# Kernel tuning notes

Hardware: AMD Instinct MI355X
Metric: run time of the kernel (lower is better)

The kernel has to match this reference:

```python
import jax, jax.numpy as jnp
import numpy as np

ALPHA = 0.2  # LeakyReLU negative slope
NEG_INF = -9e15


def setup_inputs() -> dict:
    key = jax.random.key(0)
    k1, k2, k3, k4 = jax.random.split(key, 4)
    N, F_in, F_out = 8192, 256, 64
    h = jax.random.normal(k1, (N, F_in), dtype=jnp.float32)
    adj = jax.random.randint(k2, (N, N), 0, 2, dtype=jnp.int32)
    # xavier-uniform-style scaling for params
    W = jax.random.normal(k3, (F_in, F_out), dtype=jnp.float32) * (1.0 / np.sqrt(F_in))
    a = jax.random.normal(k4, (2 * F_out, 1), dtype=jnp.float32) * (1.0 / np.sqrt(F_out))
    return {"h": h, "adj": adj, "W": W, "a": a}


def reference(h, adj, W, a):
    # Wh: [N, F_out]
    Wh = h @ W
    F_out = W.shape[1]
    a1 = a[:F_out, 0]   # attends to source (row i)
    a2 = a[F_out:, 0]   # attends to target (row j)
    f1 = Wh @ a1        # [N]
    f2 = Wh @ a2        # [N]
    # e[i, j] = leakyrelu(Wh_i . a1 + Wh_j . a2)  == original repeat/cat math
    e = jax.nn.leaky_relu(f1[:, None] + f2[None, :], negative_slope=ALPHA)
    attention = jnp.where(adj > 0, e, NEG_INF)
    attention = jax.nn.softmax(attention, axis=1)
    # dropout omitted (eval / deterministic reference)
    h_prime = attention @ Wh  # [N, F_out]
    return jax.nn.elu(h_prime)
```

## Files before the change

kernel.cpp:

```cpp
#include <hip/hip_runtime.h>
#include <hip/hip_bf16.h>
#include <stdint.h>

#define N 8192
#define FIN 256
#define FOUT 64

typedef __attribute__((ext_vector_type(8))) short s8v;
typedef __attribute__((ext_vector_type(4))) float f4v;

__device__ __forceinline__ uint32_t f2bf(float f) {
  uint32_t u = __float_as_uint(f);
  return (u + 0x7FFFu + ((u >> 16) & 1u)) >> 16;
}

__global__ __launch_bounds__(64) void gat_prep(
    const float* __restrict__ h, const float* __restrict__ W,
    const float* __restrict__ a,
    float* __restrict__ f1, float* __restrict__ f2,
    uint16_t* __restrict__ whT)
{
  const int c = threadIdx.x;
  const int i0 = blockIdx.x * 8;
  float acc[8] = {0.f, 0.f, 0.f, 0.f, 0.f, 0.f, 0.f, 0.f};
  #pragma unroll 4
  for (int k = 0; k < FIN; ++k) {
    float wv = W[k * FOUT + c];
    #pragma unroll
    for (int r = 0; r < 8; ++r)
      acc[r] += h[(size_t)(i0 + r) * FIN + k] * wv;
  }
  uint32_t b[8];
  #pragma unroll
  for (int r = 0; r < 8; ++r) b[r] = f2bf(acc[r]);
  int4 pk;
  pk.x = (int)(b[0] | (b[1] << 16));
  pk.y = (int)(b[2] | (b[3] << 16));
  pk.z = (int)(b[4] | (b[5] << 16));
  pk.w = (int)(b[6] | (b[7] << 16));
  *(int4*)(whT + (size_t)c * N + i0) = pk;

  const float a1 = a[c], a2 = a[FOUT + c];
  #pragma unroll
  for (int r = 0; r < 8; ++r) {
    float v1 = acc[r] * a1;
    float v2 = acc[r] * a2;
    #pragma unroll
    for (int m = 32; m > 0; m >>= 1) {
      v1 += __shfl_xor(v1, m, 64);
      v2 += __shfl_xor(v2, m, 64);
    }
    if (c == 0) { f1[i0 + r] = v1; f2[i0 + r] = v2; }
  }
}

__device__ __forceinline__ s8v make_afrag(float f1v, const int* __restrict__ ap,
                                          const float* __restrict__ fp, float& den) {
  int4 c0 = *(const int4*)ap;
  int4 c1 = *(const int4*)(ap + 4);
  float4 g0 = *(const float4*)fp;
  float4 g1 = *(const float4*)(fp + 4);
  float e0 = f1v + g0.x; e0 = fmaxf(e0, 0.2f * e0); float w0 = (c0.x > 0) ? __expf(e0) : 0.f;
  float e1 = f1v + g0.y; e1 = fmaxf(e1, 0.2f * e1); float w1 = (c0.y > 0) ? __expf(e1) : 0.f;
  float e2 = f1v + g0.z; e2 = fmaxf(e2, 0.2f * e2); float w2 = (c0.z > 0) ? __expf(e2) : 0.f;
  float e3 = f1v + g0.w; e3 = fmaxf(e3, 0.2f * e3); float w3 = (c0.w > 0) ? __expf(e3) : 0.f;
  float e4 = f1v + g1.x; e4 = fmaxf(e4, 0.2f * e4); float w4 = (c1.x > 0) ? __expf(e4) : 0.f;
  float e5 = f1v + g1.y; e5 = fmaxf(e5, 0.2f * e5); float w5 = (c1.y > 0) ? __expf(e5) : 0.f;
  float e6 = f1v + g1.z; e6 = fmaxf(e6, 0.2f * e6); float w6 = (c1.z > 0) ? __expf(e6) : 0.f;
  float e7 = f1v + g1.w; e7 = fmaxf(e7, 0.2f * e7); float w7 = (c1.w > 0) ? __expf(e7) : 0.f;
  uint32_t b0 = f2bf(w0), b1 = f2bf(w1), b2 = f2bf(w2), b3 = f2bf(w3);
  uint32_t b4 = f2bf(w4), b5 = f2bf(w5), b6 = f2bf(w6), b7 = f2bf(w7);
  den += __uint_as_float(b0 << 16) + __uint_as_float(b1 << 16)
       + __uint_as_float(b2 << 16) + __uint_as_float(b3 << 16)
       + __uint_as_float(b4 << 16) + __uint_as_float(b5 << 16)
       + __uint_as_float(b6 << 16) + __uint_as_float(b7 << 16);
  union { s8v v; uint32_t u[4]; } r;
  r.u[0] = b0 | (b1 << 16);
  r.u[1] = b2 | (b3 << 16);
  r.u[2] = b4 | (b5 << 16);
  r.u[3] = b6 | (b7 << 16);
  return r.v;
}

__global__ __launch_bounds__(256) void gat_main2(
    const int* __restrict__ adj, const float* __restrict__ f1,
    const float* __restrict__ f2, const uint16_t* __restrict__ whT,
    float* __restrict__ pnum, float* __restrict__ pden)
{
  const int t = threadIdx.x;
  const int wave = t >> 6;
  const int lane = t & 63;
  const int task = blockIdx.x * 4 + wave;
  const int group = task >> 2;
  const int quarter = task & 3;
  const int i0 = group * 16;
  const int jb = quarter * (N / 4);
  const int m  = lane & 15;
  const int kg = lane >> 4;

  const float f1v = f1[i0 + m];
  const int*      ap  = adj + (size_t)(i0 + m) * N + jb + kg * 8;
  const float*    fp  = f2 + jb + kg * 8;
  const uint16_t* bp0 = whT + (size_t)m * N + jb + kg * 8;

  f4v acc0 = {0.f, 0.f, 0.f, 0.f};
  f4v acc1 = acc0, acc2 = acc0, acc3 = acc0;
  float den = 0.f;

  #pragma unroll 2
  for (int jc = 0; jc < (N / 4) / 64; ++jc) {
    const int j0 = jc * 64;
    s8v a0 = make_afrag(f1v, ap + j0,      fp + j0,      den);
    s8v a1 = make_afrag(f1v, ap + j0 + 32, fp + j0 + 32, den);
    const uint16_t* bp = bp0 + j0;
    s8v b00 = *(const s8v*)(bp);
    s8v b01 = *(const s8v*)(bp + 32);
    s8v b10 = *(const s8v*)(bp + 16 * N);
    s8v b11 = *(const s8v*)(bp + 16 * N + 32);
    s8v b20 = *(const s8v*)(bp + 32 * N);
    s8v b21 = *(const s8v*)(bp + 32 * N + 32);
    s8v b30 = *(const s8v*)(bp + 48 * N);
    s8v b31 = *(const s8v*)(bp + 48 * N + 32);
    acc0 = __builtin_amdgcn_mfma_f32_16x16x32_bf16(a0, b00, acc0, 0, 0, 0);
    acc0 = __builtin_amdgcn_mfma_f32_16x16x32_bf16(a1, b01, acc0, 0, 0, 0);
    acc1 = __builtin_amdgcn_mfma_f32_16x16x32_bf16(a0, b10, acc1, 0, 0, 0);
    acc1 = __builtin_amdgcn_mfma_f32_16x16x32_bf16(a1, b11, acc1, 0, 0, 0);
    acc2 = __builtin_amdgcn_mfma_f32_16x16x32_bf16(a0, b20, acc2, 0, 0, 0);
    acc2 = __builtin_amdgcn_mfma_f32_16x16x32_bf16(a1, b21, acc2, 0, 0, 0);
    acc3 = __builtin_amdgcn_mfma_f32_16x16x32_bf16(a0, b30, acc3, 0, 0, 0);
    acc3 = __builtin_amdgcn_mfma_f32_16x16x32_bf16(a1, b31, acc3, 0, 0, 0);
  }

  den += __shfl_xor(den, 16, 64);
  den += __shfl_xor(den, 32, 64);

  float* np = pnum + (size_t)task * (16 * 64);
  #pragma unroll
  for (int r = 0; r < 4; ++r) {
    int row = kg * 4 + r;
    np[row * 64 +      m] = acc0[r];
    np[row * 64 + 16 + m] = acc1[r];
    np[row * 64 + 32 + m] = acc2[r];
    np[row * 64 + 48 + m] = acc3[r];
  }
  if (lane < 16) pden[task * 16 + m] = den;
}

__global__ __launch_bounds__(256) void gat_combine(
    const float* __restrict__ pnum, const float* __restrict__ pden,
    float* __restrict__ out)
{
  const int idx = blockIdx.x * 256 + threadIdx.x;
  const int i = idx >> 6;
  const int c = idx & 63;
  const int g = i >> 4;
  const int r = i & 15;
  const size_t base = (size_t)g * 4 * 1024 + (size_t)r * 64 + c;
  float num = pnum[base] + pnum[base + 1024] + pnum[base + 2048] + pnum[base + 3072];
  const int db = g * 64 + r;
  float den = pden[db] + pden[db + 16] + pden[db + 32] + pden[db + 48];
  float hp = num / den;
  out[idx] = (hp > 0.f) ? hp : (__expf(hp) - 1.f);
}

extern "C" void kernel_launch(void* const* d_in, const int* in_sizes, int n_in,
                              void* d_out, int out_size, void* d_ws, size_t ws_size,
                              hipStream_t stream) {
  const float* h   = (const float*)d_in[0];
  const int*   adj = (const int*)d_in[1];
  const float* W   = (const float*)d_in[2];
  const float* a   = (const float*)d_in[3];
  float* out = (float*)d_out;

  float* f1 = (float*)d_ws;
  float* f2 = f1 + N;
  uint16_t* whT = (uint16_t*)(f2 + N);
  float* pnum = (float*)(whT + (size_t)FOUT * N);
  float* pden = pnum + (size_t)2048 * 16 * 64;

  gat_prep<<<N / 8, 64, 0, stream>>>(h, W, a, f1, f2, whT);
  gat_main2<<<512, 256, 0, stream>>>(adj, f1, f2, whT, pnum, pden);
  gat_combine<<<(N * FOUT) / 256, 256, 0, stream>>>(pnum, pden, out);
}
```

Baseline: 436.9 us.

## Split column range eightfold, prefetch adjacency tiles, widen prep blocks

The main attention kernel now splits each 16-row group's column range into 8 parts instead of 4, doubling the wave count to expose more parallelism for the memory-bound adjacency stream. The adjacency and f2 loads for the next 64-column chunk are software-prefetched into registers one iteration ahead. The prep kernel moves from 64-thread blocks of 8 rows to 256-thread blocks of 4 rows per wave. Partial buffers and the combine reduction grow to 8 partials, which adds workspace traffic and register pressure.

```diff
diff --git a/kernel.cpp b/kernel.cpp
--- a/kernel.cpp
+++ b/kernel.cpp
@@ -5,6 +5,10 @@
 #define N 8192
 #define FIN 256
 #define FOUT 64
+#define QSPLIT 8
+#define NTASK (512 * QSPLIT)
+#define JLEN (N / QSPLIT)
+#define NITER (JLEN / 64)
 
 typedef __attribute__((ext_vector_type(8))) short s8v;
 typedef __attribute__((ext_vector_type(4))) float f4v;
@@ -14,35 +18,32 @@
   return (u + 0x7FFFu + ((u >> 16) & 1u)) >> 16;
 }
 
-__global__ __launch_bounds__(64) void gat_prep(
+__global__ __launch_bounds__(256) void gat_prep(
     const float* __restrict__ h, const float* __restrict__ W,
     const float* __restrict__ a,
     float* __restrict__ f1, float* __restrict__ f2,
     uint16_t* __restrict__ whT)
 {
-  const int c = threadIdx.x;
-  const int i0 = blockIdx.x * 8;
-  float acc[8] = {0.f, 0.f, 0.f, 0.f, 0.f, 0.f, 0.f, 0.f};
-  #pragma unroll 4
+  const int c = threadIdx.x & 63;
+  const int wave = threadIdx.x >> 6;
+  const int i0 = blockIdx.x * 16 + wave * 4;
+  float acc[4] = {0.f, 0.f, 0.f, 0.f};
+  #pragma unroll 8
   for (int k = 0; k < FIN; ++k) {
     float wv = W[k * FOUT + c];
     #pragma unroll
-    for (int r = 0; r < 8; ++r)
+    for (int r = 0; r < 4; ++r)
       acc[r] += h[(size_t)(i0 + r) * FIN + k] * wv;
   }
-  uint32_t b[8];
-  #pragma unroll
-  for (int r = 0; r < 8; ++r) b[r] = f2bf(acc[r]);
-  int4 pk;
-  pk.x = (int)(b[0] | (b[1] << 16));
-  pk.y = (int)(b[2] | (b[3] << 16));
-  pk.z = (int)(b[4] | (b[5] << 16));
-  pk.w = (int)(b[6] | (b[7] << 16));
-  *(int4*)(whT + (size_t)c * N + i0) = pk;
+  uint32_t b0 = f2bf(acc[0]), b1 = f2bf(acc[1]), b2 = f2bf(acc[2]), b3 = f2bf(acc[3]);
+  int2 pk;
+  pk.x = (int)(b0 | (b1 << 16));
+  pk.y = (int)(b2 | (b3 << 16));
+  *(int2*)(whT + (size_t)c * N + i0) = pk;
 
   const float a1 = a[c], a2 = a[FOUT + c];
   #pragma unroll
-  for (int r = 0; r < 8; ++r) {
+  for (int r = 0; r < 4; ++r) {
     float v1 = acc[r] * a1;
     float v2 = acc[r] * a2;
     #pragma unroll
@@ -54,12 +55,8 @@
   }
 }
 
-__device__ __forceinline__ s8v make_afrag(float f1v, const int* __restrict__ ap,
-                                          const float* __restrict__ fp, float& den) {
-  int4 c0 = *(const int4*)ap;
-  int4 c1 = *(const int4*)(ap + 4);
-  float4 g0 = *(const float4*)fp;
-  float4 g1 = *(const float4*)(fp + 4);
+__device__ __forceinline__ s8v make_afrag_r(float f1v, int4 c0, int4 c1,
+                                            float4 g0, float4 g1, float& den) {
   float e0 = f1v + g0.x; e0 = fmaxf(e0, 0.2f * e0); float w0 = (c0.x > 0) ? __expf(e0) : 0.f;
   float e1 = f1v + g0.y; e1 = fmaxf(e1, 0.2f * e1); float w1 = (c0.y > 0) ? __expf(e1) : 0.f;
   float e2 = f1v + g0.z; e2 = fmaxf(e2, 0.2f * e2); float w2 = (c0.z > 0) ? __expf(e2) : 0.f;
@@ -91,10 +88,10 @@
   const int wave = t >> 6;
   const int lane = t & 63;
   const int task = blockIdx.x * 4 + wave;
-  const int group = task >> 2;
-  const int quarter = task & 3;
+  const int group = task / QSPLIT;
+  const int quarter = task % QSPLIT;
   const int i0 = group * 16;
-  const int jb = quarter * (N / 4);
+  const int jb = quarter * JLEN;
   const int m  = lane & 15;
   const int kg = lane >> 4;
 
@@ -107,11 +104,33 @@
   f4v acc1 = acc0, acc2 = acc0, acc3 = acc0;
   float den = 0.f;
 
-  #pragma unroll 2
-  for (int jc = 0; jc < (N / 4) / 64; ++jc) {
+  int4   pc0 = *(const int4*)(ap);
+  int4   pc1 = *(const int4*)(ap + 4);
+  int4   pc2 = *(const int4*)(ap + 32);
+  int4   pc3 = *(const int4*)(ap + 36);
+  float4 pg0 = *(const float4*)(fp);
+  float4 pg1 = *(const float4*)(fp + 4);
+  float4 pg2 = *(const float4*)(fp + 32);
+  float4 pg3 = *(const float4*)(fp + 36);
+
+  #pragma unroll 1
+  for (int jc = 0; jc < NITER; ++jc) {
     const int j0 = jc * 64;
-    s8v a0 = make_afrag(f1v, ap + j0,      fp + j0,      den);
-    s8v a1 = make_afrag(f1v, ap + j0 + 32, fp + j0 + 32, den);
+    int4 c0 = pc0, c1 = pc1, c2 = pc2, c3 = pc3;
+    float4 g0 = pg0, g1 = pg1, g2 = pg2, g3 = pg3;
+    if (jc + 1 < NITER) {
+      const int jn = j0 + 64;
+      pc0 = *(const int4*)(ap + jn);
+      pc1 = *(const int4*)(ap + jn + 4);
+      pc2 = *(const int4*)(ap + jn + 32);
+      pc3 = *(const int4*)(ap + jn + 36);
+      pg0 = *(const float4*)(fp + jn);
+      pg1 = *(const float4*)(fp + jn + 4);
+      pg2 = *(const float4*)(fp + jn + 32);
+      pg3 = *(const float4*)(fp + jn + 36);
+    }
+    s8v a0 = make_afrag_r(f1v, c0, c1, g0, g1, den);
+    s8v a1 = make_afrag_r(f1v, c2, c3, g2, g3, den);
     const uint16_t* bp = bp0 + j0;
     s8v b00 = *(const s8v*)(bp);
     s8v b01 = *(const s8v*)(bp + 32);
@@ -155,10 +174,14 @@
   const int c = idx & 63;
   const int g = i >> 4;
   const int r = i & 15;
-  const size_t base = (size_t)g * 4 * 1024 + (size_t)r * 64 + c;
-  float num = pnum[base] + pnum[base + 1024] + pnum[base + 2048] + pnum[base + 3072];
-  const int db = g * 64 + r;
-  float den = pden[db] + pden[db + 16] + pden[db + 32] + pden[db + 48];
+  const size_t base = (size_t)g * QSPLIT * 1024 + (size_t)r * 64 + c;
+  float num = 0.f;
+  #pragma unroll
+  for (int q = 0; q < QSPLIT; ++q) num += pnum[base + (size_t)q * 1024];
+  const int db = g * (QSPLIT * 16) + r;
+  float den = 0.f;
+  #pragma unroll
+  for (int q = 0; q < QSPLIT; ++q) den += pden[db + q * 16];
   float hp = num / den;
   out[idx] = (hp > 0.f) ? hp : (__expf(hp) - 1.f);
 }
@@ -176,9 +199,9 @@
   float* f2 = f1 + N;
   uint16_t* whT = (uint16_t*)(f2 + N);
   float* pnum = (float*)(whT + (size_t)FOUT * N);
-  float* pden = pnum + (size_t)2048 * 16 * 64;
-
-  gat_prep<<<N / 8, 64, 0, stream>>>(h, W, a, f1, f2, whT);
-  gat_main2<<<512, 256, 0, stream>>>(adj, f1, f2, whT, pnum, pden);
+  float* pden = pnum + (size_t)NTASK * 16 * 64;
+
+  gat_prep<<<N / 16, 256, 0, stream>>>(h, W, a, f1, f2, whT);
+  gat_main2<<<NTASK / 4, 256, 0, stream>>>(adj, f1, f2, whT, pnum, pden);
   gat_combine<<<(N * FOUT) / 256, 256, 0, stream>>>(pnum, pden, out);
 }
```

Result: faster. 421.9 us (-3.4%).
